# Kernel tuning notes

Hardware: AMD Instinct MI355X
Metric: run time of the kernel (lower is better)

## Reference

```python
import jax, jax.numpy as jnp
import numpy as np

S, B, IN, H, DFF, OUT, L, NHEAD, WINDOW = 2048, 4, 64, 1024, 1024, 64, 3, 4, 4
EPS = 1e-5


def _layer_norm(x, scale, bias):
    m = jnp.mean(x, axis=-1, keepdims=True)
    v = jnp.var(x, axis=-1, keepdims=True)
    return (x - m) * jax.lax.rsqrt(v + EPS) * scale + bias


def setup_inputs() -> dict:
    key = jax.random.key(0)
    ks = jax.random.split(key, 12)
    s = 0.02
    return {
        "src": jax.random.normal(ks[0], (S, B, IN), dtype=jnp.float32),
        "Wenc": jax.random.normal(ks[1], (H, IN), dtype=jnp.float32) * s,
        "benc": jnp.zeros((H,), jnp.float32),
        "Wqkv": jax.random.normal(ks[2], (L, 3 * H, H), dtype=jnp.float32) * s,
        "bqkv": jnp.zeros((L, 3 * H), jnp.float32),
        "Wo": jax.random.normal(ks[3], (L, H, H), dtype=jnp.float32) * s,
        "bo": jnp.zeros((L, H), jnp.float32),
        "W1": jax.random.normal(ks[4], (L, DFF, H), dtype=jnp.float32) * s,
        "b1": jnp.zeros((L, DFF), jnp.float32),
        "W2": jax.random.normal(ks[5], (L, H, DFF), dtype=jnp.float32) * s,
        "b2": jnp.zeros((L, H), jnp.float32),
        "ln1_s": jnp.ones((L, H), jnp.float32),
        "ln1_b": jnp.zeros((L, H), jnp.float32),
        "ln2_s": jnp.ones((L, H), jnp.float32),
        "ln2_b": jnp.zeros((L, H), jnp.float32),
        "Wout": jax.random.normal(ks[6], (OUT, H), dtype=jnp.float32) * s,
        "bout": jnp.zeros((OUT,), jnp.float32),
    }


def _banded_mask(sz):
    # triu(1) masked + lower-band (j < i-4) masked => allowed: i-4 <= j <= i
    i = jnp.arange(sz)[:, None]
    j = jnp.arange(sz)[None, :]
    allowed = (j <= i) & (j >= i - WINDOW)
    return jnp.where(allowed, 0.0, -1e9).astype(jnp.float32)


def reference(src, Wenc, benc, Wqkv, bqkv, Wo, bo, W1, b1, W2, b2,
              ln1_s, ln1_b, ln2_s, ln2_b, Wout, bout):
    dh = H // NHEAD
    mask = _banded_mask(src.shape[0])  # [S, S]
    x = src @ Wenc.T + benc  # [S, B, H]  (NOTE: pos_encoder is never applied in the source)

    def layer(x, p):
        Wqkv_, bqkv_, Wo_, bo_, W1_, b1_, W2_, b2_, s1, g1, s2, g2 = p
        qkv = x @ Wqkv_.T + bqkv_  # [S, B, 3H]
        q, k, v = jnp.split(qkv, 3, axis=-1)
        sS, sB = x.shape[0], x.shape[1]
        q = q.reshape(sS, sB, NHEAD, dh)
        k = k.reshape(sS, sB, NHEAD, dh)
        v = v.reshape(sS, sB, NHEAD, dh)
        scores = jnp.einsum('sbhd,tbhd->bhst', q, k) / jnp.sqrt(jnp.float32(dh))
        scores = scores + mask  # broadcast over [b, h]
        attn = jax.nn.softmax(scores, axis=-1)
        ctx = jnp.einsum('bhst,tbhd->sbhd', attn, v).reshape(sS, sB, H)
        attn_out = ctx @ Wo_.T + bo_
        x = _layer_norm(x + attn_out, s1, g1)  # post-norm (PyTorch default)
        ff = jax.nn.relu(x @ W1_.T + b1_) @ W2_.T + b2_
        x = _layer_norm(x + ff, s2, g2)
        return x, None

    x, _ = jax.lax.scan(layer, x, (Wqkv, bqkv, Wo, bo, W1, b1, W2, b2,
                                   ln1_s, ln1_b, ln2_s, ln2_b))
    return x @ Wout.T + bout  # [S, B, OUT]
```

## Files before the change

kernel.cpp:

```cpp
#include <hip/hip_runtime.h>
#include <hip/hip_bf16.h>

#define S_LEN   2048
#define BATCH   4
#define IN_DIM  64
#define H_DIM   1024
#define DFF_DIM 1024
#define OUT_DIM 64
#define NLAYER  3
#define NHEADS  4
#define DHEAD   256
#define WIN     4
#define ROWS    (S_LEN*BATCH)
#define QKV_LD  (3*H_DIM)


typedef __bf16 bf16x8 __attribute__((ext_vector_type(8)));
typedef float  f32x4  __attribute__((ext_vector_type(4)));

__device__ __forceinline__ float bfbits2f(unsigned int u) {
  union { unsigned int i; float f; } c; c.i = u << 16; return c.f;
}
__device__ __forceinline__ unsigned short f2bfbits(float f) {
  __hip_bfloat16 h = __float2bfloat16(f);
  return __builtin_bit_cast(unsigned short, h);
}

__device__ __forceinline__ void g2l16(const void* g, void* l) {
  __builtin_amdgcn_global_load_lds((__attribute__((address_space(1))) void*)g,
                                   (__attribute__((address_space(3))) void*)l,
                                   16, 0, 0);
}

struct CvtSeg { const float* src; __hip_bfloat16* dst; int n4; };

__global__ __launch_bounds__(256)
void cvt_all_k(CvtSeg s0, CvtSeg s1, CvtSeg s2, CvtSeg s3,
               CvtSeg s4, CvtSeg s5, CvtSeg s6)
{
  int i = blockIdx.x * 256 + threadIdx.x;
  CvtSeg seg;
  if      (i < s0.n4) { seg = s0; }
  else if ((i -= s0.n4) < s1.n4) { seg = s1; }
  else if ((i -= s1.n4) < s2.n4) { seg = s2; }
  else if ((i -= s2.n4) < s3.n4) { seg = s3; }
  else if ((i -= s3.n4) < s4.n4) { seg = s4; }
  else if ((i -= s4.n4) < s5.n4) { seg = s5; }
  else if ((i -= s5.n4) < s6.n4) { seg = s6; }
  else return;
  float4 v = *(const float4*)(seg.src + (size_t)i * 4);
  uint2 o;
  o.x = (unsigned)f2bfbits(v.x) | ((unsigned)f2bfbits(v.y) << 16);
  o.y = (unsigned)f2bfbits(v.z) | ((unsigned)f2bfbits(v.w) << 16);
  *(uint2*)(seg.dst + (size_t)i * 4) = o;
}

template<int RELU, int OUTF32, int ADDRES>
__global__ __launch_bounds__(256, 2)
void gemm_bt(const __hip_bfloat16* __restrict__ A, int lda,
             const __hip_bfloat16* __restrict__ B,
             const float* __restrict__ bias,
             void* __restrict__ Cp, int ldc,
             const __hip_bfloat16* __restrict__ R, int ldr,
             int M, int N, int K)
{
  __shared__ __align__(16) __hip_bfloat16 As[128 * 64];
  __shared__ __align__(16) __hip_bfloat16 Bs[128 * 64];

  const int tid  = threadIdx.x;
  const int lane = tid & 63;
  const int wave = tid >> 6;
  const int quad = lane >> 4;
  const int l16  = lane & 15;

  const int gx  = gridDim.x;
  const int lin = blockIdx.y * gx + blockIdx.x;
  const int gsz = 4 * gx;
  const int mt  = (lin / gsz) * 4 + (lin & 3);
  const int nt  = (lin % gsz) >> 2;
  const int m0 = mt * 128;
  const int n0 = nt * 128;

  const int wr = (wave >> 1) * 64;
  const int wc = (wave & 1) * 64;

  int arow[4], acol[4], brow[4];
#pragma unroll
  for (int s = 0; s < 4; s++) {
    const int p = tid + (s << 8);
    arow[s] = p >> 3;
    acol[s] = ((p & 7) ^ ((p >> 3) & 7)) * 8;
    brow[s] = min(n0 + arow[s], N - 1);
  }

  f32x4 acc[4][4] = {};
  const int nk = K >> 6;

  for (int t = 0; t < nk; ++t) {
    const int k0 = t << 6;
#pragma unroll
    for (int s = 0; s < 4; s++) {
      const int lo = (wave * 64 + (s << 8)) * 8;
      g2l16(A + (size_t)(m0 + arow[s]) * lda + k0 + acol[s], &As[lo]);
      g2l16(B + (size_t)brow[s] * K + k0 + acol[s], &Bs[lo]);
    }
    __syncthreads();

#pragma unroll
    for (int kh = 0; kh < 2; kh++) {
      bf16x8 af[4], bfr[4];
#pragma unroll
      for (int i = 0; i < 4; i++) {
        const int row = wr + i * 16 + l16;
        const int c   = (kh * 4 + quad) ^ (row & 7);
        af[i] = *(const bf16x8*)&As[row * 64 + c * 8];
      }
#pragma unroll
      for (int j = 0; j < 4; j++) {
        const int row = wc + j * 16 + l16;
        const int c   = (kh * 4 + quad) ^ (row & 7);
        bfr[j] = *(const bf16x8*)&Bs[row * 64 + c * 8];
      }
#pragma unroll
      for (int i = 0; i < 4; i++)
#pragma unroll
        for (int j = 0; j < 4; j++)
          acc[i][j] = __builtin_amdgcn_mfma_f32_16x16x32_bf16(af[i], bfr[j], acc[i][j], 0, 0, 0);
    }
    __syncthreads();
  }

#pragma unroll
  for (int j = 0; j < 4; j++) {
    int col = n0 + wc + j * 16 + l16;
    if (col < N) {
      float bv = bias[col];
#pragma unroll
      for (int i = 0; i < 4; i++) {
        int row = m0 + wr + i * 16 + quad * 4;
#pragma unroll
        for (int r = 0; r < 4; r++) {
          float v = acc[i][j][r] + bv;
          if (RELU) v = fmaxf(v, 0.f);
          if (ADDRES) v += __bfloat162float(R[(size_t)(row + r) * ldr + col]);
          if (OUTF32) ((float*)Cp)[(size_t)(row + r) * ldc + col] = v;
          else ((__hip_bfloat16*)Cp)[(size_t)(row + r) * ldc + col] = __float2bfloat16(v);
        }
      }
    }
  }
}

#define ST_A(BUF, H, KO)                                                      \
  g2l16(Ab + (size_t)((H) * 64 + sarow) * lda + (KO) + sacol,                 \
        &lds[BUF][(H) << 12] + (tid << 3))
#define ST_B(BUF, H, KO)                                                      \
  do {                                                                        \
    g2l16(Bb + (size_t)((H) * 128 + sbrow) * K + (KO) + sbcol,                \
          &lds[BUF][8192 + ((H) << 13)] + (tid << 3));                        \
    g2l16(Bb + (size_t)((H) * 128 + sbrow + 64) * K + (KO) + sbcol,           \
          &lds[BUF][8192 + ((H) << 13)] + ((tid + 512) << 3));                \
  } while (0)

#define RD_AF(ASL, FRB)                                                       \
  do {                                                                        \
    _Pragma("unroll") for (int j_ = 0; j_ < 2; j_++) {                        \
      const int r_ = ((FRB) + j_) * 16 + l16;                                 \
      const int x_ = r_ & 7;                                                  \
      af[j_][0] = *(const bf16x8*)&(ASL)[r_ * 64 + ((quad ^ x_) << 3)];       \
      af[j_][1] = *(const bf16x8*)&(ASL)[r_ * 64 + (((4 + quad) ^ x_) << 3)]; \
    }                                                                         \
  } while (0)
#define RD_BQ(BSL, FCB)                                                       \
  do {                                                                        \
    _Pragma("unroll") for (int j_ = 0; j_ < 2; j_++) {                        \
      const int r_ = brow_base + ((FCB) + j_) * 16 + l16;                     \
      const int x_ = r_ & 7;                                                  \
      bq[(FCB) + j_][0] = *(const bf16x8*)&(BSL)[r_ * 64 + ((quad ^ x_) << 3)]; \
      bq[(FCB) + j_][1] = *(const bf16x8*)&(BSL)[r_ * 64 + (((4 + quad) ^ x_) << 3)]; \
    }                                                                         \
  } while (0)
#define MM(FRB, FCB)                                                          \
  do {                                                                        \
    _Pragma("unroll") for (int ks_ = 0; ks_ < 2; ks_++)                       \
      _Pragma("unroll") for (int i_ = 0; i_ < 2; i_++)                        \
        _Pragma("unroll") for (int j_ = 0; j_ < 2; j_++)                      \
          acc[(FRB) + i_][(FCB) + j_] =                                       \
              __builtin_amdgcn_mfma_f32_16x16x32_bf16(                        \
                  af[i_][ks_], bq[(FCB) + j_][ks_],                           \
                  acc[(FRB) + i_][(FCB) + j_], 0, 0, 0);                      \
  } while (0)

#define PH8(READS, STAGE, WAIT, MFMA)                                         \
  do {                                                                        \
    READS; STAGE; WAIT;                                                       \
    __builtin_amdgcn_s_barrier();                                             \
    asm volatile("s_waitcnt lgkmcnt(0)" ::: "memory");                        \
    __builtin_amdgcn_sched_barrier(0);                                        \
    __builtin_amdgcn_s_setprio(1);                                            \
    MFMA;                                                                     \
    __builtin_amdgcn_s_setprio(0);                                            \
    __builtin_amdgcn_s_barrier();                                             \
  } while (0)

#define W4CNT                                                                 \
  do {                                                                        \
    if (pf) { asm volatile("s_waitcnt vmcnt(4)" ::: "memory"); }              \
    else    { asm volatile("s_waitcnt vmcnt(0)" ::: "memory"); }              \
  } while (0)

template<int RELU, int ADDRES>
__global__ __launch_bounds__(512, 1)
void gemm8_bt(const __hip_bfloat16* __restrict__ A, int lda,
              const __hip_bfloat16* __restrict__ B,
              const float* __restrict__ bias,
              __hip_bfloat16* __restrict__ C, int ldc,
              const __hip_bfloat16* __restrict__ Rr, int ldr,
              int K)
{
  __shared__ __align__(16) __hip_bfloat16 lds[2][24576];

  const int tid  = threadIdx.x;
  const int lane = tid & 63;
  const int wave = tid >> 6;
  const int quad = lane >> 4;
  const int l16  = lane & 15;
  const int wm   = wave >> 2;
  const int wn   = wave & 3;
  const int bh   = wn >> 1;
  const int brow_base = (wn & 1) * 64;

  const int gx  = gridDim.x;
  const int lin = blockIdx.y * gx + blockIdx.x;
  const int gsz = 4 * gx;
  const int mt  = (lin / gsz) * 4 + (lin & 3);
  const int nt  = (lin % gsz) >> 2;
  const int m0 = mt * 128;
  const int n0 = nt * 256;

  const __hip_bfloat16* Ab = A + (size_t)m0 * lda;
  const __hip_bfloat16* Bb = B + (size_t)n0 * K;

  const int sarow = tid >> 3;
  const int sacol = ((tid & 7) ^ (sarow & 7)) << 3;
  const int sbrow = sarow;
  const int sbcol = sacol;

  const __hip_bfloat16* As0 = &lds[0][wm << 12];
  const __hip_bfloat16* As1 = &lds[1][wm << 12];
  const __hip_bfloat16* Bs0 = &lds[0][8192 + (bh << 13)];
  const __hip_bfloat16* Bs1 = &lds[1][8192 + (bh << 13)];

  f32x4 acc[4][4] = {};
  bf16x8 af[2][2], bq[4][2];

  const int NI = K >> 7;

  ST_A(0, 0, 0); ST_A(0, 1, 0);
  ST_B(0, 0, 0); ST_B(0, 1, 0);
  ST_B(1, 0, 64); ST_B(1, 1, 64);
  asm volatile("s_waitcnt vmcnt(4)" ::: "memory");
  __builtin_amdgcn_s_barrier();

  for (int i = 0; i < NI; ++i) {
    const int k1 = (i << 7) + 64;
    const int k2 = k1 + 64;
    const int k3 = k1 + 128;
    const bool pf = (i + 1) < NI;

    PH8(RD_AF(As0, 0); RD_BQ(Bs0, 0),  ST_A(1, 0, k1),              , MM(0, 0));
    PH8(RD_BQ(Bs0, 2),                 ST_A(1, 1, k1),              , MM(0, 2));
    PH8(RD_AF(As0, 2),                 if (pf) ST_B(0, 0, k2),      , MM(2, 0));
    PH8(                             , if (pf) ST_B(0, 1, k2), W4CNT, MM(2, 2));
    PH8(RD_AF(As1, 0); RD_BQ(Bs1, 0),  if (pf) ST_A(0, 0, k2),      , MM(0, 0));
    PH8(RD_BQ(Bs1, 2),                 if (pf) ST_A(0, 1, k2),      , MM(0, 2));
    PH8(RD_AF(As1, 2),                 if (pf) ST_B(1, 0, k3),      , MM(2, 0));
    PH8(                             , if (pf) ST_B(1, 1, k3), W4CNT, MM(2, 2));
  }

#pragma unroll
  for (int jn = 0; jn < 4; jn++) {
    const int col = n0 + wn * 64 + jn * 16 + l16;
    const float bv = bias[col];
#pragma unroll
    for (int im = 0; im < 4; im++) {
      const int row0 = m0 + wm * 64 + im * 16 + quad * 4;
      const f32x4 a = acc[im][jn];
#pragma unroll
      for (int rr = 0; rr < 4; rr++) {
        float v = a[rr] + bv;
        if (RELU) v = fmaxf(v, 0.f);
        if (ADDRES) v += __bfloat162float(Rr[(size_t)(row0 + rr) * ldr + col]);
        C[(size_t)(row0 + rr) * ldc + col] = __float2bfloat16(v);
      }
    }
  }
}

__global__ __launch_bounds__(256)
void attn_k(__hip_bfloat16* __restrict__ qkv)
{
  const int gw   = (blockIdx.x << 2) + (threadIdx.x >> 6);
  const int lane = threadIdx.x & 63;
  const int h = gw & (NHEADS - 1);
  const int b = (gw >> 2) & (BATCH - 1);
  const int s = gw >> 4;
  const size_t hoff = (size_t)h * DHEAD + (lane << 2);

  float q0, q1, q2, q3;
  {
    uint2 t = *(const uint2*)(qkv + (size_t)(s * BATCH + b) * QKV_LD + hoff);
    q0 = bfbits2f(t.x & 0xffff); q1 = bfbits2f(t.x >> 16);
    q2 = bfbits2f(t.y & 0xffff); q3 = bfbits2f(t.y >> 16);
  }

  float sc[WIN + 1];
#pragma unroll
  for (int jj = 0; jj <= WIN; jj++) {
    int j = s - WIN + jj;
    float v = -1e30f;
    if (j >= 0) {
      uint2 t = *(const uint2*)(qkv + (size_t)(j * BATCH + b) * QKV_LD + H_DIM + hoff);
      float p = q0 * bfbits2f(t.x & 0xffff) + q1 * bfbits2f(t.x >> 16)
              + q2 * bfbits2f(t.y & 0xffff) + q3 * bfbits2f(t.y >> 16);
#pragma unroll
      for (int o = 32; o; o >>= 1) p += __shfl_xor(p, o);
      v = p * 0.0625f;
    }
    sc[jj] = v;
  }

  float mx = sc[0];
#pragma unroll
  for (int jj = 1; jj <= WIN; jj++) mx = fmaxf(mx, sc[jj]);
  float p[WIN + 1], den = 0.f;
#pragma unroll
  for (int jj = 0; jj <= WIN; jj++) { p[jj] = __expf(sc[jj] - mx); den += p[jj]; }

  float a0 = 0.f, a1 = 0.f, a2 = 0.f, a3 = 0.f;
#pragma unroll
  for (int jj = 0; jj <= WIN; jj++) {
    int j = s - WIN + jj;
    if (j >= 0) {
      uint2 t = *(const uint2*)(qkv + (size_t)(j * BATCH + b) * QKV_LD + 2 * H_DIM + hoff);
      a0 += p[jj] * bfbits2f(t.x & 0xffff); a1 += p[jj] * bfbits2f(t.x >> 16);
      a2 += p[jj] * bfbits2f(t.y & 0xffff); a3 += p[jj] * bfbits2f(t.y >> 16);
    }
  }
  float rl = 1.f / den;
  uint2 o;
  o.x = (unsigned)f2bfbits(a0 * rl) | ((unsigned)f2bfbits(a1 * rl) << 16);
  o.y = (unsigned)f2bfbits(a2 * rl) | ((unsigned)f2bfbits(a3 * rl) << 16);
  *(uint2*)(qkv + (size_t)(s * BATCH + b) * QKV_LD + hoff) = o;
}

__global__ __launch_bounds__(256)
void ln_k(const __hip_bfloat16* __restrict__ y, int ys,
          const float* __restrict__ g, const float* __restrict__ be,
          __hip_bfloat16* __restrict__ xout)
{
  const int row  = blockIdx.x * 4 + (threadIdx.x >> 6);
  const int lane = threadIdx.x & 63;
  const int e0   = lane * 16;
  const __hip_bfloat16* yp = y + (size_t)row * ys + e0;

  uint2 v[4];
  *(uint4*)&v[0] = *(const uint4*)yp;
  *(uint4*)&v[2] = *(const uint4*)(yp + 8);
  float t[16];
#pragma unroll
  for (int k = 0; k < 4; k++) {
    t[k * 4 + 0] = bfbits2f(v[k].x & 0xffff);
    t[k * 4 + 1] = bfbits2f(v[k].x >> 16);
    t[k * 4 + 2] = bfbits2f(v[k].y & 0xffff);
    t[k * 4 + 3] = bfbits2f(v[k].y >> 16);
  }
  float s = 0.f, ss = 0.f;
#pragma unroll
  for (int k = 0; k < 16; k++) { s += t[k]; ss += t[k] * t[k]; }
#pragma unroll
  for (int o = 32; o; o >>= 1) { s += __shfl_xor(s, o); ss += __shfl_xor(ss, o); }

  const float inv  = 1.f / (float)H_DIM;
  const float mean = s * inv;
  const float var  = ss * inv - mean * mean;
  const float rstd = rsqrtf(var + 1e-5f);

  float4 gv[4], bv[4];
#pragma unroll
  for (int k = 0; k < 4; k++) {
    gv[k] = *(const float4*)(g + e0 + k * 4);
    bv[k] = *(const float4*)(be + e0 + k * 4);
  }
  uint2 ob[4];
#pragma unroll
  for (int k = 0; k < 4; k++) {
    float o0 = (t[k*4+0] - mean) * rstd * gv[k].x + bv[k].x;
    float o1 = (t[k*4+1] - mean) * rstd * gv[k].y + bv[k].y;
    float o2 = (t[k*4+2] - mean) * rstd * gv[k].z + bv[k].z;
    float o3 = (t[k*4+3] - mean) * rstd * gv[k].w + bv[k].w;
    ob[k].x = (unsigned)f2bfbits(o0) | ((unsigned)f2bfbits(o1) << 16);
    ob[k].y = (unsigned)f2bfbits(o2) | ((unsigned)f2bfbits(o3) << 16);
  }
  __hip_bfloat16* xp = xout + (size_t)row * H_DIM + e0;
  *(uint4*)xp       = *(const uint4*)&ob[0];
  *(uint4*)(xp + 8) = *(const uint4*)&ob[2];
}

extern "C" void kernel_launch(void* const* d_in, const int* in_sizes, int n_in,
                              void* d_out, int out_size, void* d_ws, size_t ws_size,
                              hipStream_t stream) {
  const float* src   = (const float*)d_in[0];
  const float* Wenc  = (const float*)d_in[1];
  const float* benc  = (const float*)d_in[2];
  const float* Wqkv  = (const float*)d_in[3];
  const float* bqkv  = (const float*)d_in[4];
  const float* Wo    = (const float*)d_in[5];
  const float* bo    = (const float*)d_in[6];
  const float* W1    = (const float*)d_in[7];
  const float* b1    = (const float*)d_in[8];
  const float* W2    = (const float*)d_in[9];
  const float* b2    = (const float*)d_in[10];
  const float* ln1s  = (const float*)d_in[11];
  const float* ln1b  = (const float*)d_in[12];
  const float* ln2s  = (const float*)d_in[13];
  const float* ln2b  = (const float*)d_in[14];
  const float* Wout  = (const float*)d_in[15];
  const float* bout  = (const float*)d_in[16];

  char* ws = (char*)d_ws;
  __hip_bfloat16* WB   = (__hip_bfloat16*)ws;
  __hip_bfloat16* srcb = WB;
  __hip_bfloat16* wenc = WB + 524288;
  __hip_bfloat16* wqkv = WB + 589824;
  __hip_bfloat16* wo   = WB + 10027008;
  __hip_bfloat16* w1   = WB + 13172736;
  __hip_bfloat16* w2   = WB + 16318464;
  __hip_bfloat16* wout = WB + 19464192;
  __hip_bfloat16* xb  = (__hip_bfloat16*)(ws + (size_t)40 * 1048576);
  __hip_bfloat16* qkv = (__hip_bfloat16*)(ws + (size_t)56 * 1048576);
  __hip_bfloat16* ctxp = qkv;
  __hip_bfloat16* ybuf = qkv + H_DIM;
  __hip_bfloat16* hbuf = qkv + 2 * H_DIM;

  const dim3 blk(256);
  const dim3 blk512(512);

  {
    CvtSeg s0{src,  srcb, 524288 / 4};
    CvtSeg s1{Wenc, wenc, 65536 / 4};
    CvtSeg s2{Wqkv, wqkv, 9437184 / 4};
    CvtSeg s3{Wo,   wo,   3145728 / 4};
    CvtSeg s4{W1,   w1,   3145728 / 4};
    CvtSeg s5{W2,   w2,   3145728 / 4};
    CvtSeg s6{Wout, wout, 65536 / 4};
    const int tot4 = (524288 + 65536 + 9437184 + 3 * 3145728 + 65536) / 4;
    cvt_all_k<<<dim3((tot4 + 255) / 256), blk, 0, stream>>>(s0, s1, s2, s3, s4, s5, s6);
  }

  gemm_bt<0, 0, 0><<<dim3(H_DIM / 128, ROWS / 128), blk, 0, stream>>>(
      srcb, IN_DIM, wenc, benc, xb, H_DIM, nullptr, 0, ROWS, H_DIM, IN_DIM);

  for (int l = 0; l < NLAYER; l++) {
    gemm8_bt<0, 0><<<dim3(QKV_LD / 256, ROWS / 128), blk512, 0, stream>>>(
        xb, H_DIM, wqkv + (size_t)l * QKV_LD * H_DIM, bqkv + l * QKV_LD,
        qkv, QKV_LD, nullptr, 0, H_DIM);
    attn_k<<<dim3(ROWS * NHEADS / 4), blk, 0, stream>>>(qkv);
    gemm8_bt<0, 1><<<dim3(H_DIM / 256, ROWS / 128), blk512, 0, stream>>>(
        ctxp, QKV_LD, wo + (size_t)l * H_DIM * H_DIM, bo + l * H_DIM,
        ybuf, QKV_LD, xb, H_DIM, H_DIM);
    ln_k<<<dim3(ROWS / 4), blk, 0, stream>>>(ybuf, QKV_LD, ln1s + l * H_DIM, ln1b + l * H_DIM, xb);
    gemm8_bt<1, 0><<<dim3(DFF_DIM / 256, ROWS / 128), blk512, 0, stream>>>(
        xb, H_DIM, w1 + (size_t)l * DFF_DIM * H_DIM, b1 + l * DFF_DIM,
        hbuf, QKV_LD, nullptr, 0, H_DIM);
    gemm8_bt<0, 1><<<dim3(H_DIM / 256, ROWS / 128), blk512, 0, stream>>>(
        hbuf, QKV_LD, w2 + (size_t)l * H_DIM * DFF_DIM, b2 + l * H_DIM,
        ybuf, QKV_LD, xb, H_DIM, DFF_DIM);
    ln_k<<<dim3(ROWS / 4), blk, 0, stream>>>(ybuf, QKV_LD, ln2s + l * H_DIM, ln2b + l * H_DIM, xb);
  }

  gemm_bt<0, 1, 0><<<dim3(1, ROWS / 128), blk, 0, stream>>>(
      xb, H_DIM, wout, bout, d_out, OUT_DIM, nullptr, 0, ROWS, OUT_DIM, H_DIM);
}
```

Baseline: 699.1 us.

## Add 256x256-tile GEMM kernel for the QKV projection

Introduces gemm256_bt, a 512-thread GEMM with 256x256 output tiles, double-buffered 128 KB LDS, swizzled layout and an 8-phase MFMA pipeline. Each wave now computes 128x64. The QKV projection switches to it, halving the number of M tiles and raising arithmetic intensity per byte loaded. In exchange, occupancy drops to one block per CU, register pressure rises, and the grid shrinks to 384 blocks, which may hurt load balance on the CUs.

```diff
diff --git a/kernel.cpp b/kernel.cpp
--- a/kernel.cpp
+++ b/kernel.cpp
@@ -285,6 +285,135 @@
 #pragma unroll
     for (int im = 0; im < 4; im++) {
       const int row0 = m0 + wm * 64 + im * 16 + quad * 4;
+      const f32x4 a = acc[im][jn];
+#pragma unroll
+      for (int rr = 0; rr < 4; rr++) {
+        float v = a[rr] + bv;
+        if (RELU) v = fmaxf(v, 0.f);
+        if (ADDRES) v += __bfloat162float(Rr[(size_t)(row0 + rr) * ldr + col]);
+        C[(size_t)(row0 + rr) * ldc + col] = __float2bfloat16(v);
+      }
+    }
+  }
+}
+
+#define S6_A(BUF, H, KO)                                                      \
+  do {                                                                        \
+    g2l16(Ab + (size_t)((H) * 128 + srow) * lda + (KO) + scol,                \
+          &lds6[BUF][(H) << 13] + (tid << 3));                                \
+    g2l16(Ab + (size_t)((H) * 128 + srow + 64) * lda + (KO) + scol,           \
+          &lds6[BUF][(H) << 13] + ((tid + 512) << 3));                        \
+  } while (0)
+#define S6_B(BUF, H, KO)                                                      \
+  do {                                                                        \
+    g2l16(Bb + (size_t)((H) * 128 + srow) * K + (KO) + scol,                  \
+          &lds6[BUF][16384 + ((H) << 13)] + (tid << 3));                      \
+    g2l16(Bb + (size_t)((H) * 128 + srow + 64) * K + (KO) + scol,             \
+          &lds6[BUF][16384 + ((H) << 13)] + ((tid + 512) << 3));              \
+  } while (0)
+
+#define R6_A(ASL, FIB)                                                        \
+  do {                                                                        \
+    _Pragma("unroll") for (int i_ = 0; i_ < 4; i_++) {                        \
+      const int r_ = ((FIB) + i_) * 16 + l16;                                 \
+      const int x_ = r_ & 7;                                                  \
+      af[i_][0] = *(const bf16x8*)&(ASL)[r_ * 64 + ((quad ^ x_) << 3)];       \
+      af[i_][1] = *(const bf16x8*)&(ASL)[r_ * 64 + (((4 + quad) ^ x_) << 3)]; \
+    }                                                                         \
+  } while (0)
+#define R6_B(BSL, FJB)                                                        \
+  do {                                                                        \
+    _Pragma("unroll") for (int j_ = 0; j_ < 2; j_++) {                        \
+      const int r_ = brow_base + ((FJB) + j_) * 16 + l16;                     \
+      const int x_ = r_ & 7;                                                  \
+      bq[(FJB) + j_][0] = *(const bf16x8*)&(BSL)[r_ * 64 + ((quad ^ x_) << 3)]; \
+      bq[(FJB) + j_][1] = *(const bf16x8*)&(BSL)[r_ * 64 + (((4 + quad) ^ x_) << 3)]; \
+    }                                                                         \
+  } while (0)
+#define M6(FIB, FJB)                                                          \
+  do {                                                                        \
+    _Pragma("unroll") for (int ks_ = 0; ks_ < 2; ks_++)                       \
+      _Pragma("unroll") for (int i_ = 0; i_ < 4; i_++)                        \
+        _Pragma("unroll") for (int j_ = 0; j_ < 2; j_++)                      \
+          acc[(FIB) + i_][(FJB) + j_] =                                       \
+              __builtin_amdgcn_mfma_f32_16x16x32_bf16(                        \
+                  af[i_][ks_], bq[(FJB) + j_][ks_],                           \
+                  acc[(FIB) + i_][(FJB) + j_], 0, 0, 0);                      \
+  } while (0)
+
+template<int RELU, int ADDRES>
+__global__ __launch_bounds__(512, 1)
+void gemm256_bt(const __hip_bfloat16* __restrict__ A, int lda,
+                const __hip_bfloat16* __restrict__ B,
+                const float* __restrict__ bias,
+                __hip_bfloat16* __restrict__ C, int ldc,
+                const __hip_bfloat16* __restrict__ Rr, int ldr,
+                int K)
+{
+  __shared__ __align__(16) __hip_bfloat16 lds6[2][32768];
+
+  const int tid  = threadIdx.x;
+  const int lane = tid & 63;
+  const int wave = tid >> 6;
+  const int quad = lane >> 4;
+  const int l16  = lane & 15;
+  const int wm   = wave >> 2;
+  const int wn   = wave & 3;
+  const int brow_base = (wn & 1) * 64;
+
+  const int gx  = gridDim.x;
+  const int lin = blockIdx.y * gx + blockIdx.x;
+  const int gsz = 4 * gx;
+  const int mt  = (lin / gsz) * 4 + (lin & 3);
+  const int nt  = (lin % gsz) >> 2;
+  const int m0 = mt * 256;
+  const int n0 = nt * 256;
+
+  const __hip_bfloat16* Ab = A + (size_t)m0 * lda;
+  const __hip_bfloat16* Bb = B + (size_t)n0 * K;
+
+  const int srow = tid >> 3;
+  const int scol = ((tid & 7) ^ (srow & 7)) << 3;
+
+  const __hip_bfloat16* As0 = &lds6[0][wm << 13];
+  const __hip_bfloat16* As1 = &lds6[1][wm << 13];
+  const __hip_bfloat16* Bs0 = &lds6[0][16384 + ((wn >> 1) << 13)];
+  const __hip_bfloat16* Bs1 = &lds6[1][16384 + ((wn >> 1) << 13)];
+
+  f32x4 acc[8][4] = {};
+  bf16x8 af[4][2], bq[4][2];
+
+  const int NI = K >> 7;
+
+  S6_A(0, 0, 0); S6_A(0, 1, 0);
+  S6_B(0, 0, 0); S6_B(0, 1, 0);
+  S6_B(1, 0, 64); S6_B(1, 1, 64);
+  asm volatile("s_waitcnt vmcnt(4)" ::: "memory");
+  __builtin_amdgcn_s_barrier();
+
+  for (int i = 0; i < NI; ++i) {
+    const int k1 = (i << 7) + 64;
+    const int k2 = k1 + 64;
+    const int k3 = k1 + 128;
+    const bool pf = (i + 1) < NI;
+
+    PH8(R6_A(As0, 0); R6_B(Bs0, 0),  S6_A(1, 0, k1),              , M6(0, 0));
+    PH8(R6_B(Bs0, 2),                S6_A(1, 1, k1),              , M6(0, 2));
+    PH8(R6_A(As0, 4),                if (pf) S6_B(0, 0, k2),      , M6(4, 0));
+    PH8(                           , if (pf) S6_B(0, 1, k2), W4CNT, M6(4, 2));
+    PH8(R6_A(As1, 0); R6_B(Bs1, 0),  if (pf) S6_A(0, 0, k2),      , M6(0, 0));
+    PH8(R6_B(Bs1, 2),                if (pf) S6_A(0, 1, k2),      , M6(0, 2));
+    PH8(R6_A(As1, 4),                if (pf) S6_B(1, 0, k3),      , M6(4, 0));
+    PH8(                           , if (pf) S6_B(1, 1, k3), W4CNT, M6(4, 2));
+  }
+
+#pragma unroll
+  for (int jn = 0; jn < 4; jn++) {
+    const int col = n0 + wn * 64 + jn * 16 + l16;
+    const float bv = bias[col];
+#pragma unroll
+    for (int im = 0; im < 8; im++) {
+      const int row0 = m0 + wm * 128 + im * 16 + quad * 4;
       const f32x4 a = acc[im][jn];
 #pragma unroll
       for (int rr = 0; rr < 4; rr++) {
@@ -462,7 +591,7 @@
       srcb, IN_DIM, wenc, benc, xb, H_DIM, nullptr, 0, ROWS, H_DIM, IN_DIM);
 
   for (int l = 0; l < NLAYER; l++) {
-    gemm8_bt<0, 0><<<dim3(QKV_LD / 256, ROWS / 128), blk512, 0, stream>>>(
+    gemm256_bt<0, 0><<<dim3(QKV_LD / 256, ROWS / 256), blk512, 0, stream>>>(
         xb, H_DIM, wqkv + (size_t)l * QKV_LD * H_DIM, bqkv + l * QKV_LD,
         qkv, QKV_LD, nullptr, 0, H_DIM);
     attn_k<<<dim3(ROWS * NHEADS / 4), blk, 0, stream>>>(qkv);
```

After: 701.5 us. No clear change (+0.4%).
